# Performance work log

Hardware: AMD Instinct MI355X
Metric: run time of the kernel (lower is better)

The kernel has to match this reference:

```python
import jax, jax.numpy as jnp
import numpy as np

N_NODES = 20000
N_EDGES = 640000
IN_DIM = 128
HID = 128
NUM_GRAPHS = 64


def setup_inputs() -> dict:
    key = jax.random.key(0)
    ks = jax.random.split(key, 12)
    x = jax.random.normal(ks[0], (N_NODES, IN_DIM), dtype=jnp.float32)
    edge_index = jax.random.randint(ks[1], (2, N_EDGES), 0, N_NODES, dtype=jnp.int64)
    batch = jnp.sort(jax.random.randint(ks[2], (N_NODES,), 0, NUM_GRAPHS, dtype=jnp.int64))
    edge_attr = jax.random.uniform(ks[3], (N_EDGES,), dtype=jnp.float32)
    s1 = 1.0 / np.sqrt(IN_DIM)
    s2 = 1.0 / np.sqrt(HID)
    # GraphConv layer 1: lin_rel (with bias) on aggregated messages, lin_root (no bias) on x
    W1_rel = jax.random.uniform(ks[4], (HID, IN_DIM), minval=-s1, maxval=s1, dtype=jnp.float32)
    b1 = jax.random.uniform(ks[5], (HID,), minval=-s1, maxval=s1, dtype=jnp.float32)
    W1_root = jax.random.uniform(ks[6], (HID, IN_DIM), minval=-s1, maxval=s1, dtype=jnp.float32)
    # GraphConv layer 3 (conv2 is unused in forward)
    W3_rel = jax.random.uniform(ks[7], (HID, HID), minval=-s2, maxval=s2, dtype=jnp.float32)
    b3 = jax.random.uniform(ks[8], (HID,), minval=-s2, maxval=s2, dtype=jnp.float32)
    W3_root = jax.random.uniform(ks[9], (HID, HID), minval=-s2, maxval=s2, dtype=jnp.float32)
    # Final linear head
    Wlin = jax.random.uniform(ks[10], (1, HID), minval=-s2, maxval=s2, dtype=jnp.float32)
    blin = jax.random.uniform(ks[11], (1,), minval=-s2, maxval=s2, dtype=jnp.float32)
    return {
        "x": x, "edge_index": edge_index, "batch": batch, "edge_attr": edge_attr,
        "W1_rel": W1_rel, "b1": b1, "W1_root": W1_root,
        "W3_rel": W3_rel, "b3": b3, "W3_root": W3_root,
        "Wlin": Wlin, "blin": blin, "num_graphs": NUM_GRAPHS,
    }


def graph_conv(x, src, dst, edge_w, W_rel, b_rel, W_root):
    # PyG GraphConv (aggr='add'): out = W_rel @ sum_{j in N(i)} w_ij * x_j + b_rel + W_root @ x_i
    msg = x[src] * edge_w[:, None]                       # [E, d] gather + scale
    agg = jax.ops.segment_sum(msg, dst, num_segments=x.shape[0])  # [N, d] scatter-add
    return agg @ W_rel.T + b_rel + x @ W_root.T


def reference(x, edge_index, batch, edge_attr,
              W1_rel, b1, W1_root, W3_rel, b3, W3_root, Wlin, blin, num_graphs):
    src, dst = edge_index[0], edge_index[1]
    h = graph_conv(x, src, dst, edge_attr, W1_rel, b1, W1_root)
    h = jax.nn.relu(h)
    # dropout p=0.5 is identity in eval mode
    h = graph_conv(h, src, dst, edge_attr, W3_rel, b3, W3_root)
    # global_mean_pool over per-node graph ids
    sums = jax.ops.segment_sum(h, batch, num_segments=num_graphs)          # [G, H]
    counts = jax.ops.segment_sum(jnp.ones((h.shape[0],), h.dtype), batch,
                                 num_segments=num_graphs)                  # [G]
    pooled = sums / jnp.maximum(counts, 1.0)[:, None]
    out = jax.nn.relu(pooled @ Wlin.T + blin)                              # [G, 1]
    return out
```

## Files before the change

### kernel.cpp

```cpp
#include <hip/hip_runtime.h>

#define N_NODES 20000
#define N_EDGES 640000
#define DIM 128
#define NGRAPH 64
#define NBUCK 313
#define EPB 2048
#define NB_CONV 256
#define NB_HIST 313
#define NB_WCONV 32
#define RED_BLOCKS 512

typedef __attribute__((ext_vector_type(8))) short short8;
typedef __attribute__((ext_vector_type(4))) float floatx4;

__device__ __forceinline__ unsigned int bf16rne(float f) {
    unsigned int u = __float_as_uint(f);
    return (u + 0x7FFFu + ((u >> 16) & 1u)) >> 16;
}

__global__ __launch_bounds__(256) void k_front(
    const float* __restrict__ x, const int* __restrict__ dst,
    const float* __restrict__ Wrel, const float* __restrict__ Wroot,
    const float* __restrict__ W3rel, const float* __restrict__ W3root,
    const float* __restrict__ b3, const float* __restrict__ Wlin,
    unsigned short* __restrict__ xbh, unsigned short* __restrict__ xbl,
    unsigned short* __restrict__ wbh, unsigned short* __restrict__ wbl,
    int* __restrict__ ghist, int* __restrict__ ticket_hist,
    int* __restrict__ boff, int* __restrict__ gcursor,
    float* __restrict__ vrel, float* __restrict__ vroot, float* __restrict__ cb3) {

    const int t = threadIdx.x;
    const int blk = blockIdx.x;

    if (blk < NB_CONV) {
        const float4* x4 = (const float4*)x;
        uint2* xh2 = (uint2*)xbh;
        uint2* xl2 = (uint2*)xbl;
        for (int i = blk * 256 + t; i < N_NODES * 32; i += NB_CONV * 256) {
            float4 v = x4[i];
            unsigned int h0 = bf16rne(v.x), h1 = bf16rne(v.y);
            unsigned int h2 = bf16rne(v.z), h3 = bf16rne(v.w);
            float l0 = v.x - __uint_as_float(h0 << 16);
            float l1 = v.y - __uint_as_float(h1 << 16);
            float l2 = v.z - __uint_as_float(h2 << 16);
            float l3 = v.w - __uint_as_float(h3 << 16);
            uint2 hp, lp;
            hp.x = h0 | (h1 << 16);
            hp.y = h2 | (h3 << 16);
            lp.x = bf16rne(l0) | (bf16rne(l1) << 16);
            lp.y = bf16rne(l2) | (bf16rne(l3) << 16);
            xh2[i] = hp;
            xl2[i] = lp;
        }
    } else if (blk < NB_CONV + NB_HIST) {
        __shared__ int lhist[NBUCK];
        __shared__ int islast;
        const int hb = blk - NB_CONV;
        for (int i = t; i < NBUCK; i += 256) lhist[i] = 0;
        __syncthreads();
        const int e0 = hb * EPB;
        for (int i = 0; i < 8; ++i) {
            int e = e0 + i * 256 + t;
            if (e < N_EDGES) atomicAdd(&lhist[dst[e] >> 6], 1);
        }
        __syncthreads();
        for (int i = t; i < NBUCK; i += 256)
            if (lhist[i]) atomicAdd(&ghist[i], lhist[i]);
        __syncthreads();
        if (t == 0) {
            __threadfence();
            islast = (atomicAdd(ticket_hist, 1) == NB_HIST - 1);
        }
        __syncthreads();
        if (islast) {
            __threadfence();
            if (t < 64) {
                int carry = 0;
                for (int c = 0; c < 5; ++c) {
                    int idx = c * 64 + t;
                    int v = (idx < NBUCK)
                        ? __hip_atomic_load(&ghist[idx], __ATOMIC_RELAXED,
                                            __HIP_MEMORY_SCOPE_AGENT)
                        : 0;
                    int xv = v;
                    for (int s = 1; s < 64; s <<= 1) {
                        int u = __shfl_up(xv, s);
                        if (t >= s) xv += u;
                    }
                    int excl = carry + xv - v;
                    if (idx < NBUCK) { boff[idx] = excl; gcursor[idx] = excl; }
                    carry += __shfl(xv, 63);
                }
                if (t == 0) boff[NBUCK] = carry;
            }
        }
    } else if (blk < NB_CONV + NB_HIST + NB_WCONV) {
        const int b = blk - (NB_CONV + NB_HIST);
        for (int i = b * 256 + t; i < 256 * DIM; i += NB_WCONV * 256) {
            int n = i >> 7, k = i & 127;
            float v = (n < DIM) ? Wrel[n * DIM + k] : Wroot[(n - DIM) * DIM + k];
            unsigned int h = bf16rne(v);
            wbh[i] = (unsigned short)h;
            wbl[i] = (unsigned short)bf16rne(v - __uint_as_float(h << 16));
        }
    } else {
        if (t < 64) {
            for (int kk = 0; kk < 2; ++kk) {
                int k = t + kk * 64;
                float sr = 0.f, so = 0.f;
                for (int h = 0; h < DIM; ++h) {
                    float wl = Wlin[h];
                    sr = fmaf(wl, W3rel[h * DIM + k], sr);
                    so = fmaf(wl, W3root[h * DIM + k], so);
                }
                vrel[k] = sr;
                vroot[k] = so;
            }
            float c = b3[t] * Wlin[t] + b3[t + 64] * Wlin[t + 64];
            for (int m = 32; m > 0; m >>= 1) c += __shfl_xor(c, m);
            if (t == 0) cb3[0] = c;
        }
    }
}

__global__ __launch_bounds__(256) void k_partition(const int* __restrict__ src,
                                                   const int* __restrict__ dst,
                                                   const float* __restrict__ ew,
                                                   int* __restrict__ gcursor,
                                                   int2* __restrict__ part) {
    __shared__ int lhist[NBUCK], gbase[NBUCK], lcur[NBUCK];
    const int t = threadIdx.x;
    for (int i = t; i < NBUCK; i += 256) lhist[i] = 0;
    __syncthreads();
    const int e0 = blockIdx.x * EPB;
    int mys[8], myd[8];
    float myw[8];
    for (int i = 0; i < 8; ++i) {
        int e = e0 + i * 256 + t;
        if (e < N_EDGES) {
            mys[i] = src[e];
            myd[i] = dst[e];
            myw[i] = ew[e];
            atomicAdd(&lhist[myd[i] >> 6], 1);
        } else {
            myd[i] = -1;
        }
    }
    __syncthreads();
    for (int i = t; i < NBUCK; i += 256) {
        gbase[i] = lhist[i] ? atomicAdd(&gcursor[i], lhist[i]) : 0;
        lcur[i] = 0;
    }
    __syncthreads();
    for (int i = 0; i < 8; ++i) {
        if (myd[i] >= 0) {
            int b = myd[i] >> 6;
            int rk = atomicAdd(&lcur[b], 1);
            part[gbase[b] + rk] =
                make_int2(((myd[i] & 63) << 16) | mys[i], __float_as_int(myw[i]));
        }
    }
}

__global__ __launch_bounds__(256) void k_gemm(
    const unsigned short* __restrict__ xbh, const unsigned short* __restrict__ xbl,
    const unsigned short* __restrict__ wbh, const unsigned short* __restrict__ wbl,
    const float* __restrict__ b1,
    unsigned short* __restrict__ yb, float* __restrict__ r) {
    extern __shared__ unsigned short smem[];
    uint4* sh = (uint4*)smem;
    uint4* sl = (uint4*)(smem + 16384);

    const int t = threadIdx.x;
    const int g = blockIdx.x;
    const int half = blockIdx.y;
    const int n0 = half * 128;

    const uint4* gh = (const uint4*)wbh + (size_t)n0 * 16;
    const uint4* gl = (const uint4*)wbl + (size_t)n0 * 16;
    for (int i = t; i < 2048; i += 256) {
        int row = i >> 4, c = i & 15;
        int sc = row * 16 + (c ^ (row & 15));
        sh[sc] = gh[i];
        sl[sc] = gl[i];
    }
    __syncthreads();

    const int lane = t & 63;
    const int m = lane & 15;
    const int q = lane >> 4;
    const int row0 = g * 64 + (t >> 6) * 16;
    const int arow = (row0 + m) * 16 + q;

    const short8* Ah = (const short8*)xbh;
    const short8* Al = (const short8*)xbl;
    const short8* SH = (const short8*)smem;
    const short8* SL = (const short8*)(smem + 16384);

    floatx4 acc[8];
    #pragma unroll
    for (int i = 0; i < 8; ++i) acc[i] = (floatx4)(0.f);

    #pragma unroll
    for (int kc = 0; kc < 4; ++kc) {
        short8 ah = Ah[arow + kc * 4];
        short8 al = Al[arow + kc * 4];
        #pragma unroll
        for (int nt = 0; nt < 8; ++nt) {
            int n = nt * 16 + m;
            int cc = (kc * 4 + q) ^ m;
            short8 bh = SH[n * 16 + cc];
            short8 bl = SL[n * 16 + cc];
            acc[nt] = __builtin_amdgcn_mfma_f32_16x16x32_bf16(ah, bh, acc[nt], 0, 0, 0);
            acc[nt] = __builtin_amdgcn_mfma_f32_16x16x32_bf16(al, bh, acc[nt], 0, 0, 0);
            acc[nt] = __builtin_amdgcn_mfma_f32_16x16x32_bf16(ah, bl, acc[nt], 0, 0, 0);
        }
    }

    #pragma unroll
    for (int nt = 0; nt < 8; ++nt) {
        int col = n0 + nt * 16 + m;
        float bias = (col >= DIM) ? b1[col - DIM] : 0.f;
        #pragma unroll
        for (int reg = 0; reg < 4; ++reg) {
            int row = row0 + q * 4 + reg;
            if (row < N_NODES) {
                float v = acc[nt][reg];
                if (col < DIM)
                    yb[row * DIM + col] = (unsigned short)bf16rne(v);
                else
                    r[row * DIM + (col - DIM)] = v + bias;
            }
        }
    }
}

__global__ __launch_bounds__(256) void k_bucketsort(const int* __restrict__ boff,
                                                    const int2* __restrict__ part,
                                                    int2* __restrict__ sorted,
                                                    int* __restrict__ off) {
    __shared__ int nh[64], ncur[64];
    const int b = blockIdx.x;
    const int t = threadIdx.x;
    const int s0 = boff[b], s1 = boff[b + 1];
    if (t < 64) nh[t] = 0;
    __syncthreads();
    for (int i = s0 + t; i < s1; i += 256) atomicAdd(&nh[part[i].x >> 16], 1);
    __syncthreads();
    if (t < 64) {
        int v = nh[t];
        int xv = v;
        for (int s = 1; s < 64; s <<= 1) {
            int u = __shfl_up(xv, s);
            if (t >= s) xv += u;
        }
        int excl = xv - v;
        ncur[t] = excl;
        int node = b * 64 + t;
        if (node < N_NODES) off[node] = s0 + excl;
    }
    __syncthreads();
    for (int i = s0 + t; i < s1; i += 256) {
        int2 rc = part[i];
        int dl = rc.x >> 16;
        int p = atomicAdd(&ncur[dl], 1);
        sorted[s0 + p] = make_int2(rc.x & 0xFFFF, rc.y);
    }
    if (b == 0 && t == 0) off[N_NODES] = N_EDGES;
}

__global__ __launch_bounds__(256) void k_agg(const unsigned int* __restrict__ yb,
                                             const float2* __restrict__ r2,
                                             const int* __restrict__ off,
                                             const int2* __restrict__ grec,
                                             const float2* __restrict__ vrel2,
                                             const float2* __restrict__ vroot2,
                                             float* __restrict__ aout,
                                             float* __restrict__ bout) {
    const int lane = threadIdx.x & 63;
    const int node = blockIdx.x * 4 + (threadIdx.x >> 6);
    if (node >= N_NODES) return;

    int j = off[node];
    const int e1 = off[node + 1];
    float sx = 0.f, sy = 0.f;
    for (; j + 4 <= e1; j += 4) {
        int2 r0 = grec[j], r1 = grec[j + 1], rr2 = grec[j + 2], r3 = grec[j + 3];
        float w0 = __int_as_float(r0.y), w1 = __int_as_float(r1.y);
        float w2 = __int_as_float(rr2.y), w3 = __int_as_float(r3.y);
        unsigned int v0 = yb[r0.x * 64 + lane];
        unsigned int v1 = yb[r1.x * 64 + lane];
        unsigned int v2 = yb[rr2.x * 64 + lane];
        unsigned int v3 = yb[r3.x * 64 + lane];
        sx = fmaf(w0, __uint_as_float(v0 << 16),
             fmaf(w1, __uint_as_float(v1 << 16),
             fmaf(w2, __uint_as_float(v2 << 16),
             fmaf(w3, __uint_as_float(v3 << 16), sx))));
        sy = fmaf(w0, __uint_as_float(v0 & 0xFFFF0000u),
             fmaf(w1, __uint_as_float(v1 & 0xFFFF0000u),
             fmaf(w2, __uint_as_float(v2 & 0xFFFF0000u),
             fmaf(w3, __uint_as_float(v3 & 0xFFFF0000u), sy))));
    }
    for (; j < e1; ++j) {
        int2 rc = grec[j];
        float w = __int_as_float(rc.y);
        unsigned int v = yb[rc.x * 64 + lane];
        sx = fmaf(w, __uint_as_float(v << 16), sx);
        sy = fmaf(w, __uint_as_float(v & 0xFFFF0000u), sy);
    }
    float2 rr = r2[node * 64 + lane];
    float hx = fmaxf(sx + rr.x, 0.f);
    float hy = fmaxf(sy + rr.y, 0.f);
    float2 vr = vrel2[lane];
    float2 vo = vroot2[lane];
    float pa = hx * vr.x + hy * vr.y;
    float pb = hx * vo.x + hy * vo.y;
    for (int mm = 32; mm > 0; mm >>= 1) {
        pa += __shfl_xor(pa, mm);
        pb += __shfl_xor(pb, mm);
    }
    if (lane == 0) {
        aout[node] = pa;
        bout[node] = pb;
    }
}

__global__ __launch_bounds__(256) void k_reduce_final(
    const int2* __restrict__ sorted, const int* __restrict__ off,
    const float* __restrict__ a, const float* __restrict__ bvec,
    const int* __restrict__ batch,
    float* __restrict__ gpart, int* __restrict__ gpartc,
    int* __restrict__ ticket_red,
    const float* __restrict__ cb3, const float* __restrict__ blin,
    float* __restrict__ out) {
    __shared__ float sbin[NGRAPH];
    __shared__ int cbin[NGRAPH];
    __shared__ int islast;
    const int t = threadIdx.x;
    for (int i = t; i < NGRAPH; i += 256) { sbin[i] = 0.f; cbin[i] = 0; }
    __syncthreads();
    const int lane = t & 63;
    const int gw = blockIdx.x * 4 + (t >> 6);
    const int nw = gridDim.x * 4;
    for (int node = gw; node < N_NODES; node += nw) {
        const int e0 = off[node], e1 = off[node + 1];
        float s = 0.f;
        for (int j = e0 + lane; j < e1; j += 64) {
            int2 rc = sorted[j];
            s = fmaf(__int_as_float(rc.y), a[rc.x], s);
        }
        for (int mm = 32; mm > 0; mm >>= 1) s += __shfl_xor(s, mm);
        if (lane == 0) {
            int g = batch[node];
            atomicAdd(&sbin[g], s + bvec[node]);
            atomicAdd(&cbin[g], 1);
        }
    }
    __syncthreads();
    const int slot = blockIdx.x & 63;
    for (int i = t; i < NGRAPH; i += 256) {
        atomicAdd(&gpart[slot * NGRAPH + i], sbin[i]);
        if (cbin[i]) atomicAdd(&gpartc[slot * NGRAPH + i], cbin[i]);
    }
    __syncthreads();
    if (t == 0) {
        __threadfence();
        islast = (atomicAdd(ticket_red, 1) == (int)gridDim.x - 1);
    }
    __syncthreads();
    if (islast) {
        __threadfence();
        if (t < NGRAPH) {
            float S = 0.f;
            int C = 0;
            for (int s2 = 0; s2 < 64; ++s2) {
                S += __hip_atomic_load(&gpart[s2 * NGRAPH + t], __ATOMIC_RELAXED,
                                       __HIP_MEMORY_SCOPE_AGENT);
                C += __hip_atomic_load(&gpartc[s2 * NGRAPH + t], __ATOMIC_RELAXED,
                                       __HIP_MEMORY_SCOPE_AGENT);
            }
            float denom = (C > 0) ? (float)C : 1.f;
            float v = (S + (float)C * cb3[0]) / denom + blin[0];
            out[t] = (v > 0.f) ? v : 0.f;
        }
    }
}

extern "C" void kernel_launch(void* const* d_in, const int* in_sizes, int n_in,
                              void* d_out, int out_size, void* d_ws, size_t ws_size,
                              hipStream_t stream) {
    const float* x = (const float*)d_in[0];
    const int* edge_index = (const int*)d_in[1];
    const int* src = edge_index;
    const int* dst = edge_index + N_EDGES;
    const int* batch = (const int*)d_in[2];
    const float* ew = (const float*)d_in[3];
    const float* W1rel = (const float*)d_in[4];
    const float* b1 = (const float*)d_in[5];
    const float* W1root = (const float*)d_in[6];
    const float* W3rel = (const float*)d_in[7];
    const float* b3 = (const float*)d_in[8];
    const float* W3root = (const float*)d_in[9];
    const float* Wlin = (const float*)d_in[10];
    const float* blin = (const float*)d_in[11];
    float* out = (float*)d_out;

    char* w = (char*)d_ws;
    size_t o = 0;
    auto alloc = [&](size_t bytes) -> void* {
        void* p = w + o;
        o += bytes;
        o = (o + 255) & ~(size_t)255;
        return p;
    };
    char* zbase = (char*)alloc(1280 + 64 * NGRAPH * 4 * 2);
    int* ghist = (int*)zbase;
    int* ticket_hist = ghist + NBUCK;
    int* ticket_red = ghist + NBUCK + 1;
    float* gpart = (float*)(zbase + 1280);
    int* gpartc = (int*)(zbase + 1280 + 64 * NGRAPH * 4);
    const size_t zbytes = 1280 + 64 * NGRAPH * 4 * 2;

    unsigned short* xbh = (unsigned short*)alloc((size_t)20032 * DIM * 2);
    unsigned short* xbl = (unsigned short*)alloc((size_t)20032 * DIM * 2);
    unsigned short* wbh = (unsigned short*)alloc((size_t)256 * DIM * 2);
    unsigned short* wbl = (unsigned short*)alloc((size_t)256 * DIM * 2);
    unsigned short* yb = (unsigned short*)alloc((size_t)N_NODES * DIM * 2);
    float* r = (float*)alloc((size_t)N_NODES * DIM * 4);
    int* boff = (int*)alloc((size_t)(NBUCK + 1) * 4);
    int* gcursor = (int*)alloc((size_t)NBUCK * 4);
    int2* part = (int2*)alloc((size_t)N_EDGES * 8);
    int2* sorted = (int2*)alloc((size_t)N_EDGES * 8);
    int* off = (int*)alloc((size_t)(N_NODES + 1) * 4);
    float* a = (float*)alloc((size_t)N_NODES * 4);
    float* b = (float*)alloc((size_t)N_NODES * 4);
    float* vrel = (float*)alloc(DIM * 4);
    float* vroot = (float*)alloc(DIM * 4);
    float* cb3 = (float*)alloc(4);

    hipMemsetAsync(zbase, 0, zbytes, stream);

    k_front<<<NB_CONV + NB_HIST + NB_WCONV + 1, 256, 0, stream>>>(
        x, dst, W1rel, W1root, W3rel, W3root, b3, Wlin,
        xbh, xbl, wbh, wbl, ghist, ticket_hist, boff, gcursor,
        vrel, vroot, cb3);

    k_partition<<<NB_HIST, 256, 0, stream>>>(src, dst, ew, gcursor, part);

    k_gemm<<<dim3(NBUCK, 2), 256, 65536, stream>>>(
        xbh, xbl, wbh, wbl, b1, yb, r);

    k_bucketsort<<<NBUCK, 256, 0, stream>>>(boff, part, sorted, off);

    k_agg<<<(N_NODES + 3) / 4, 256, 0, stream>>>(
        (const unsigned int*)yb, (const float2*)r, off, sorted,
        (const float2*)vrel, (const float2*)vroot, a, b);

    k_reduce_final<<<RED_BLOCKS, 256, 0, stream>>>(
        sorted, off, a, b, batch, gpart, gpartc, ticket_red, cb3, blin, out);
}
```

Measured before the change: 196.1 us.

## Fuse x bf16 split into GEMM and stage partition writes in LDS

Drops the separate pass that converts x into high/low bf16 arrays. The GEMM now loads fp32 x directly and does the split in registers, which removes a 20000x128 round trip through memory. The partition kernel now groups its records by bucket in shared memory before writing them out, so global writes within each bucket are contiguous. The cost is that the two GEMM column-half blocks each redo the conversion, and the partition kernel uses more LDS and an extra barrier.

```diff
diff --git a/kernel.cpp b/kernel.cpp
--- a/kernel.cpp
+++ b/kernel.cpp
@@ -6,7 +6,6 @@
 #define NGRAPH 64
 #define NBUCK 313
 #define EPB 2048
-#define NB_CONV 256
 #define NB_HIST 313
 #define NB_WCONV 32
 #define RED_BLOCKS 512
@@ -20,11 +19,10 @@
 }
 
 __global__ __launch_bounds__(256) void k_front(
-    const float* __restrict__ x, const int* __restrict__ dst,
+    const int* __restrict__ dst,
     const float* __restrict__ Wrel, const float* __restrict__ Wroot,
     const float* __restrict__ W3rel, const float* __restrict__ W3root,
     const float* __restrict__ b3, const float* __restrict__ Wlin,
-    unsigned short* __restrict__ xbh, unsigned short* __restrict__ xbl,
     unsigned short* __restrict__ wbh, unsigned short* __restrict__ wbl,
     int* __restrict__ ghist, int* __restrict__ ticket_hist,
     int* __restrict__ boff, int* __restrict__ gcursor,
@@ -33,33 +31,12 @@
     const int t = threadIdx.x;
     const int blk = blockIdx.x;
 
-    if (blk < NB_CONV) {
-        const float4* x4 = (const float4*)x;
-        uint2* xh2 = (uint2*)xbh;
-        uint2* xl2 = (uint2*)xbl;
-        for (int i = blk * 256 + t; i < N_NODES * 32; i += NB_CONV * 256) {
-            float4 v = x4[i];
-            unsigned int h0 = bf16rne(v.x), h1 = bf16rne(v.y);
-            unsigned int h2 = bf16rne(v.z), h3 = bf16rne(v.w);
-            float l0 = v.x - __uint_as_float(h0 << 16);
-            float l1 = v.y - __uint_as_float(h1 << 16);
-            float l2 = v.z - __uint_as_float(h2 << 16);
-            float l3 = v.w - __uint_as_float(h3 << 16);
-            uint2 hp, lp;
-            hp.x = h0 | (h1 << 16);
-            hp.y = h2 | (h3 << 16);
-            lp.x = bf16rne(l0) | (bf16rne(l1) << 16);
-            lp.y = bf16rne(l2) | (bf16rne(l3) << 16);
-            xh2[i] = hp;
-            xl2[i] = lp;
-        }
-    } else if (blk < NB_CONV + NB_HIST) {
+    if (blk < NB_HIST) {
         __shared__ int lhist[NBUCK];
         __shared__ int islast;
-        const int hb = blk - NB_CONV;
         for (int i = t; i < NBUCK; i += 256) lhist[i] = 0;
         __syncthreads();
-        const int e0 = hb * EPB;
+        const int e0 = blk * EPB;
         for (int i = 0; i < 8; ++i) {
             int e = e0 + i * 256 + t;
             if (e < N_EDGES) atomicAdd(&lhist[dst[e] >> 6], 1);
@@ -95,8 +72,8 @@
                 if (t == 0) boff[NBUCK] = carry;
             }
         }
-    } else if (blk < NB_CONV + NB_HIST + NB_WCONV) {
-        const int b = blk - (NB_CONV + NB_HIST);
+    } else if (blk < NB_HIST + NB_WCONV) {
+        const int b = blk - NB_HIST;
         for (int i = b * 256 + t; i < 256 * DIM; i += NB_WCONV * 256) {
             int n = i >> 7, k = i & 127;
             float v = (n < DIM) ? Wrel[n * DIM + k] : Wroot[(n - DIM) * DIM + k];
@@ -129,11 +106,13 @@
                                                    const float* __restrict__ ew,
                                                    int* __restrict__ gcursor,
                                                    int2* __restrict__ part) {
-    __shared__ int lhist[NBUCK], gbase[NBUCK], lcur[NBUCK];
+    __shared__ int lhist[NBUCK], lbase[NBUCK], gbase[NBUCK], lcur[NBUCK];
+    __shared__ int2 lrec[EPB];
     const int t = threadIdx.x;
     for (int i = t; i < NBUCK; i += 256) lhist[i] = 0;
     __syncthreads();
     const int e0 = blockIdx.x * EPB;
+    const int tot = min(EPB, N_EDGES - e0);
     int mys[8], myd[8];
     float myw[8];
     for (int i = 0; i < 8; ++i) {
@@ -148,23 +127,43 @@
         }
     }
     __syncthreads();
+    if (t < 64) {
+        int carry = 0;
+        for (int c = 0; c < 5; ++c) {
+            int idx = c * 64 + t;
+            int v = (idx < NBUCK) ? lhist[idx] : 0;
+            int xv = v;
+            for (int s = 1; s < 64; s <<= 1) {
+                int u = __shfl_up(xv, s);
+                if (t >= s) xv += u;
+            }
+            if (idx < NBUCK) { lbase[idx] = carry + xv - v; lcur[idx] = 0; }
+            carry += __shfl(xv, 63);
+        }
+    }
+    __syncthreads();
     for (int i = t; i < NBUCK; i += 256) {
-        gbase[i] = lhist[i] ? atomicAdd(&gcursor[i], lhist[i]) : 0;
-        lcur[i] = 0;
+        int cnt = lhist[i];
+        gbase[i] = cnt ? atomicAdd(&gcursor[i], cnt) : 0;
     }
     __syncthreads();
     for (int i = 0; i < 8; ++i) {
         if (myd[i] >= 0) {
-            int b = myd[i] >> 6;
-            int rk = atomicAdd(&lcur[b], 1);
-            part[gbase[b] + rk] =
-                make_int2(((myd[i] & 63) << 16) | mys[i], __float_as_int(myw[i]));
-        }
+            int bb = myd[i] >> 6;
+            int slot = lbase[bb] + atomicAdd(&lcur[bb], 1);
+            lrec[slot] = make_int2((myd[i] << 16) | mys[i], __float_as_int(myw[i]));
+        }
+    }
+    __syncthreads();
+    for (int i = t; i < tot; i += 256) {
+        int2 rc = lrec[i];
+        int bb = (rc.x >> 16) >> 6;
+        part[gbase[bb] + (i - lbase[bb])] = rc;
     }
 }
 
 __global__ __launch_bounds__(256) void k_gemm(
-    const unsigned short* __restrict__ xbh, const unsigned short* __restrict__ xbl,
+    const float* __restrict__ x,
     const unsigned short* __restrict__ wbh, const unsigned short* __restrict__ wbl,
     const float* __restrict__ b1,
     unsigned short* __restrict__ yb, float* __restrict__ r) {
@@ -191,10 +190,9 @@
     const int m = lane & 15;
     const int q = lane >> 4;
     const int row0 = g * 64 + (t >> 6) * 16;
-    const int arow = (row0 + m) * 16 + q;
-
-    const short8* Ah = (const short8*)xbh;
-    const short8* Al = (const short8*)xbl;
+    const int row = row0 + m;
+    const bool ok = row < N_NODES;
+
     const short8* SH = (const short8*)smem;
     const short8* SL = (const short8*)(smem + 16384);
 
@@ -204,8 +202,21 @@
 
     #pragma unroll
     for (int kc = 0; kc < 4; ++kc) {
-        short8 ah = Ah[arow + kc * 4];
-        short8 al = Al[arow + kc * 4];
+        float4 v0 = make_float4(0.f, 0.f, 0.f, 0.f);
+        float4 v1 = make_float4(0.f, 0.f, 0.f, 0.f);
+        if (ok) {
+            const float4* xp = (const float4*)(x + (size_t)row * DIM + kc * 32 + q * 8);
+            v0 = xp[0];
+            v1 = xp[1];
+        }
+        float f[8] = {v0.x, v0.y, v0.z, v0.w, v1.x, v1.y, v1.z, v1.w};
+        short8 ah, al;
+        #pragma unroll
+        for (int i = 0; i < 8; ++i) {
+            unsigned int h = bf16rne(f[i]);
+            ah[i] = (short)h;
+            al[i] = (short)bf16rne(f[i] - __uint_as_float(h << 16));
+        }
         #pragma unroll
         for (int nt = 0; nt < 8; ++nt) {
             int n = nt * 16 + m;
@@ -224,13 +235,13 @@
         float bias = (col >= DIM) ? b1[col - DIM] : 0.f;
         #pragma unroll
         for (int reg = 0; reg < 4; ++reg) {
-            int row = row0 + q * 4 + reg;
-            if (row < N_NODES) {
+            int orow = row0 + q * 4 + reg;
+            if (orow < N_NODES) {
                 float v = acc[nt][reg];
                 if (col < DIM)
-                    yb[row * DIM + col] = (unsigned short)bf16rne(v);
+                    yb[orow * DIM + col] = (unsigned short)bf16rne(v);
                 else
-                    r[row * DIM + (col - DIM)] = v + bias;
+                    r[orow * DIM + (col - DIM)] = v + bias;
             }
         }
     }
@@ -246,7 +257,7 @@
     const int s0 = boff[b], s1 = boff[b + 1];
     if (t < 64) nh[t] = 0;
     __syncthreads();
-    for (int i = s0 + t; i < s1; i += 256) atomicAdd(&nh[part[i].x >> 16], 1);
+    for (int i = s0 + t; i < s1; i += 256) atomicAdd(&nh[(part[i].x >> 16) & 63], 1);
     __syncthreads();
     if (t < 64) {
         int v = nh[t];
@@ -263,7 +274,7 @@
     __syncthreads();
     for (int i = s0 + t; i < s1; i += 256) {
         int2 rc = part[i];
-        int dl = rc.x >> 16;
+        int dl = (rc.x >> 16) & 63;
         int p = atomicAdd(&ncur[dl], 1);
         sorted[s0 + p] = make_int2(rc.x & 0xFFFF, rc.y);
     }
@@ -309,7 +320,7 @@
         sx = fmaf(w, __uint_as_float(v << 16), sx);
         sy = fmaf(w, __uint_as_float(v & 0xFFFF0000u), sy);
     }
-    float2 rr = r2[node * 64 + lane];
+    float2 rr = r2[(size_t)node * 64 + lane];
     float hx = fmaxf(sx + rr.x, 0.f);
     float hy = fmaxf(sy + rr.y, 0.f);
     float2 vr = vrel2[lane];
@@ -422,8 +433,6 @@
     int* gpartc = (int*)(zbase + 1280 + 64 * NGRAPH * 4);
     const size_t zbytes = 1280 + 64 * NGRAPH * 4 * 2;
 
-    unsigned short* xbh = (unsigned short*)alloc((size_t)20032 * DIM * 2);
-    unsigned short* xbl = (unsigned short*)alloc((size_t)20032 * DIM * 2);
     unsigned short* wbh = (unsigned short*)alloc((size_t)256 * DIM * 2);
     unsigned short* wbl = (unsigned short*)alloc((size_t)256 * DIM * 2);
     unsigned short* yb = (unsigned short*)alloc((size_t)N_NODES * DIM * 2);
@@ -441,15 +450,13 @@
 
     hipMemsetAsync(zbase, 0, zbytes, stream);
 
-    k_front<<<NB_CONV + NB_HIST + NB_WCONV + 1, 256, 0, stream>>>(
-        x, dst, W1rel, W1root, W3rel, W3root, b3, Wlin,
-        xbh, xbl, wbh, wbl, ghist, ticket_hist, boff, gcursor,
-        vrel, vroot, cb3);
+    k_front<<<NB_HIST + NB_WCONV + 1, 256, 0, stream>>>(
+        dst, W1rel, W1root, W3rel, W3root, b3, Wlin,
+        wbh, wbl, ghist, ticket_hist, boff, gcursor, vrel, vroot, cb3);
 
     k_partition<<<NB_HIST, 256, 0, stream>>>(src, dst, ew, gcursor, part);
 
-    k_gemm<<<dim3(NBUCK, 2), 256, 65536, stream>>>(
-        xbh, xbl, wbh, wbl, b1, yb, r);
+    k_gemm<<<dim3(NBUCK, 2), 256, 65536, stream>>>(x, wbh, wbl, b1, yb, r);
 
     k_bucketsort<<<NBUCK, 256, 0, stream>>>(boff, part, sorted, off);
 
```

Result: no change. 194.4 us (-0.9%).
